# Performance work log

Measured on AMD Instinct MI355X. Metric: run time of the kernel, lower is better.

## Reference

```python
import jax, jax.numpy as jnp
import numpy as np

T, H, I, E, K, L, R = 1024, 1024, 1024, 8, 2, 4, 16
N = 2 * I  # gate_up dim


def setup_inputs() -> dict:
    key = jax.random.key(0)
    ks = jax.random.split(key, 12)
    tw = jax.random.uniform(ks[1], (T, K), dtype=jnp.float32) + 0.1
    tw = tw / tw.sum(axis=-1, keepdims=True)  # routing weights sum to 1
    return {
        "hidden_states": jax.random.normal(ks[0], (T, H), dtype=jnp.float32),
        "topk_weights": tw,
        "w13": jax.random.normal(ks[2], (E, N, H), dtype=jnp.float32) * (1.0 / np.sqrt(H)),
        "w2": jax.random.normal(ks[3], (E, H, I), dtype=jnp.float32) * (1.0 / np.sqrt(I)),
        "gate_up_lora_a": jax.random.normal(ks[4], (L, E, R, H), dtype=jnp.float32) * (1.0 / np.sqrt(H)),
        "gate_up_lora_b": jax.random.normal(ks[5], (L, E, N, R), dtype=jnp.float32) * (1.0 / np.sqrt(R)),
        "down_lora_a": jax.random.normal(ks[6], (L, E, R, I), dtype=jnp.float32) * (1.0 / np.sqrt(I)),
        "down_lora_b": jax.random.normal(ks[7], (L, E, H, R), dtype=jnp.float32) * (1.0 / np.sqrt(R)),
        "scalings": jax.random.uniform(ks[8], (L,), dtype=jnp.float32) + 0.5,
        "topk_ids": jax.random.randint(ks[9], (T, K), 0, E, dtype=jnp.int32),
        "lora_indices": jax.random.randint(ks[10], (T,), 0, L, dtype=jnp.int32),
    }


def reference(hidden_states, topk_weights, w13, w2, gate_up_lora_a,
              gate_up_lora_b, down_lora_a, down_lora_b, scalings,
              topk_ids, lora_indices):
    num_tokens, hidden = hidden_states.shape
    num_experts, gate_up_dim, _ = w13.shape
    top_k = topk_ids.shape[1]
    inter = gate_up_dim // 2
    TKp = num_tokens * top_k

    e_flat = topk_ids.reshape(-1)                      # [TK] expert per dispatched pair
    l_flat = jnp.repeat(lora_indices, top_k)           # [TK] adapter per pair
    w_flat = topk_weights.reshape(-1)                  # [TK] routing weight
    x_rep = jnp.repeat(hidden_states, top_k, axis=0)   # [TK, H]

    # ---- grouped gate_up GEMM (base path): cache1[p] = x[p] @ w13[e(p)]^T ----
    cache1 = jnp.zeros((TKp, gate_up_dim), dtype=hidden_states.dtype)
    for ei in range(num_experts):  # small fixed expert count
        mask = (e_flat == ei)[:, None]
        cache1 = cache1 + jnp.where(mask, x_rep @ w13[ei].T, 0.0)

    # ---- per-expert gate_up LoRA delta, injected BEFORE activation ----
    scal = scalings[l_flat][:, None]                   # [TK, 1]
    Ag = gate_up_lora_a[l_flat, e_flat]                # [TK, R, H]
    Bg = gate_up_lora_b[l_flat, e_flat]                # [TK, N, R]
    tmp = jnp.einsum('prh,ph->pr', Ag, x_rep)
    cache1 = cache1 + jnp.einsum('pnr,pr->pn', Bg, tmp) * scal

    # ---- silu_and_mul on (base + lora) ----
    act = jax.nn.silu(cache1[:, :inter]) * cache1[:, inter:]   # [TK, I]

    # ---- grouped down GEMM (base), routed-weight applied ----
    cache3 = jnp.zeros((TKp, hidden), dtype=hidden_states.dtype)
    for ei in range(num_experts):
        mask = (e_flat == ei)[:, None]
        cache3 = cache3 + jnp.where(mask, act @ w2[ei].T, 0.0)
    cache3 = cache3 * w_flat[:, None]

    # ---- per-expert down LoRA delta (weighted by routing weight) ----
    Ad = down_lora_a[l_flat, e_flat]                   # [TK, R, I]
    Bd = down_lora_b[l_flat, e_flat]                   # [TK, H, R]
    tmpd = jnp.einsum('pri,pi->pr', Ad, act)
    cache3 = cache3 + jnp.einsum('phr,pr->ph', Bd, tmpd) * scal * w_flat[:, None]

    # ---- combine expert outputs (moe_sum over top_k slots) ----
    return cache3.reshape(num_tokens, top_k, hidden).sum(axis=1)
```

## Files before the change

kernel.cpp:

```cpp
#include <hip/hip_runtime.h>
#include <stdint.h>

#define Td 1024
#define Hd 1024
#define Id 1024
#define Ed 8
#define Kd 2
#define Ld 4
#define Rd 16
#define Nd 2048
#define TKd (Td*Kd)

typedef __bf16 bf16x8 __attribute__((ext_vector_type(8)));
typedef float f32x4 __attribute__((ext_vector_type(4)));

__device__ __forceinline__ ushort f2bf(float f) {
    uint32_t u = __builtin_bit_cast(uint32_t, f);
    return (ushort)((u + 0x7fffu + ((u >> 16) & 1u)) >> 16);
}
__device__ __forceinline__ float bf2f(ushort u) {
    uint32_t x = ((uint32_t)u) << 16;
    return __builtin_bit_cast(float, x);
}
__device__ __forceinline__ bf16x8 pack8(float4 a, float4 b) {
    bf16x8 r;
    r[0] = (__bf16)a.x; r[1] = (__bf16)a.y; r[2] = (__bf16)a.z; r[3] = (__bf16)a.w;
    r[4] = (__bf16)b.x; r[5] = (__bf16)b.y; r[6] = (__bf16)b.z; r[7] = (__bf16)b.w;
    return r;
}
__device__ __forceinline__ void cvt16(const float* __restrict__ s, ushort* __restrict__ d) {
    float4 a0 = *(const float4*)(s);
    float4 a1 = *(const float4*)(s + 4);
    float4 a2 = *(const float4*)(s + 8);
    float4 a3 = *(const float4*)(s + 12);
    uint4 o0, o1;
    o0.x = (uint)f2bf(a0.x) | ((uint)f2bf(a0.y) << 16);
    o0.y = (uint)f2bf(a0.z) | ((uint)f2bf(a0.w) << 16);
    o0.z = (uint)f2bf(a1.x) | ((uint)f2bf(a1.y) << 16);
    o0.w = (uint)f2bf(a1.z) | ((uint)f2bf(a1.w) << 16);
    o1.x = (uint)f2bf(a2.x) | ((uint)f2bf(a2.y) << 16);
    o1.y = (uint)f2bf(a2.z) | ((uint)f2bf(a2.w) << 16);
    o1.z = (uint)f2bf(a3.x) | ((uint)f2bf(a3.y) << 16);
    o1.w = (uint)f2bf(a3.z) | ((uint)f2bf(a3.w) << 16);
    *(uint4*)(d) = o0;
    *(uint4*)(d + 8) = o1;
}

#define GLOAD_LDS16(g, l) __builtin_amdgcn_global_load_lds( \
    (const __attribute__((address_space(1))) uint32_t*)(const void*)(g), \
    (__attribute__((address_space(3))) uint32_t*)(void*)(l), 16, 0, 0)

__device__ __forceinline__ int xcd_swz(int bid, int tot) {
    int q = tot >> 3, r = tot & 7;
    int x = bid & 7, i = bid >> 3;
    return (x < r) ? x * (q + 1) + i : r * (q + 1) + (x - r) * q + i;
}

#define TB 2048
#define XB 256
#define CB 384
#define ZB 1024
#define PREP_BLOCKS (TB + XB + CB + ZB + 1)

__global__ __launch_bounds__(256) void k_prep(
    const float* __restrict__ hid,
    const float* __restrict__ gb, const float* __restrict__ db,
    const float* __restrict__ ga, const float* __restrict__ sc,
    const int* __restrict__ tids, const int* __restrict__ lidx,
    ushort* __restrict__ xb,
    ushort* __restrict__ gbbe, ushort* __restrict__ dbbe, ushort* __restrict__ tmp1e,
    float* __restrict__ out, int* __restrict__ sorted, int* __restrict__ offs)
{
    __shared__ float tr[Rd];
    __shared__ int cnt[Ed];
    __shared__ int cur[Ed];
    const int b = blockIdx.x, tid = threadIdx.x;

    if (b < TB) {
        const int p = b;
        const int e = tids[p];
        const int l = lidx[p >> 1];
        const float s = sc[l];
        const int r = tid >> 4, q = tid & 15;
        const float* A = ga + (((size_t)l * Ed + e) * Rd + r) * 1024;
        const float* x = hid + (size_t)(p >> 1) * 1024;
        float sum = 0.f;
        #pragma unroll
        for (int i = 0; i < 16; ++i) {
            int h = q * 4 + 64 * i;
            float4 a = *(const float4*)(A + h);
            float4 v = *(const float4*)(x + h);
            sum += a.x * v.x + a.y * v.y + a.z * v.z + a.w * v.w;
        }
        sum += __shfl_xor(sum, 1); sum += __shfl_xor(sum, 2);
        sum += __shfl_xor(sum, 4); sum += __shfl_xor(sum, 8);
        if (q == 0) tr[r] = sum;
        __syncthreads();
        if (tid < 32) {
            int j0 = tid * 2;
            uint v = 0;
            if ((j0 >> 4) == l)
                v = (uint)f2bf(s * tr[j0 & 15]) | ((uint)f2bf(s * tr[(j0 + 1) & 15]) << 16);
            ((uint*)(tmp1e + (size_t)p * 64))[tid] = v;
        }
    } else if (b < TB + XB) {
        size_t off = ((size_t)(b - TB) * 256 + tid) * 16;
        cvt16(hid + off, xb + off);
    } else if (b < TB + XB + CB) {
        constexpr int GR = Ld * Ed * Nd;
        int i = (b - TB - XB) * 256 + tid;
        const float* src; ushort* dst;
        if (i < GR) {
            int l = i >> 14, e = (i >> 11) & 7, n = i & 2047;
            src = gb + (size_t)i * 16;
            dst = gbbe + ((size_t)(e * Nd + n)) * 64 + l * 16;
        } else {
            int j = i - GR;
            int l = j >> 13, e = (j >> 10) & 7, n = j & 1023;
            src = db + (size_t)j * 16;
            dst = dbbe + ((size_t)(e * Id + n)) * 64 + l * 16;
        }
        cvt16(src, dst);
    } else if (b < TB + XB + CB + ZB) {
        int i = (b - TB - XB - CB) * 256 + tid;
        ((float4*)out)[i] = make_float4(0.f, 0.f, 0.f, 0.f);
    } else {
        if (tid < Ed) cnt[tid] = 0;
        __syncthreads();
        int el[8];
        #pragma unroll
        for (int i = 0; i < 8; ++i) {
            el[i] = tids[tid + i * 256];
            atomicAdd(&cnt[el[i]], 1);
        }
        __syncthreads();
        if (tid == 0) {
            int s = 0;
            for (int e = 0; e < Ed; ++e) { offs[e] = s; cur[e] = s; s += cnt[e]; }
            offs[Ed] = s;
        }
        __syncthreads();
        #pragma unroll
        for (int i = 0; i < 8; ++i) {
            int pos = atomicAdd(&cur[el[i]], 1);
            sorted[pos] = tid + i * 256;
        }
    }
}

__global__ __launch_bounds__(256) void k_tmp_dn(
    const ushort* __restrict__ act, const float* __restrict__ da,
    const float* __restrict__ sc, const int* __restrict__ tids,
    const int* __restrict__ lidx, ushort* __restrict__ tmpde)
{
    const int p = blockIdx.x;
    const int e = tids[p];
    const int l = lidx[p >> 1];
    const float s = sc[l];
    const int tid = threadIdx.x;
    const int r = tid >> 4, q = tid & 15;
    const float* A = da + (((size_t)l * Ed + e) * Rd + r) * 1024;
    const ushort* x = act + (size_t)p * 1024;
    float sum = 0.f;
    #pragma unroll
    for (int i = 0; i < 8; ++i) {
        int h = q * 8 + 128 * i;
        float4 a0 = *(const float4*)(A + h);
        float4 a1 = *(const float4*)(A + h + 4);
        ushort4 v0 = *(const ushort4*)(x + h);
        ushort4 v1 = *(const ushort4*)(x + h + 4);
        sum += a0.x * bf2f(v0.x) + a0.y * bf2f(v0.y) + a0.z * bf2f(v0.z) + a0.w * bf2f(v0.w)
             + a1.x * bf2f(v1.x) + a1.y * bf2f(v1.y) + a1.z * bf2f(v1.z) + a1.w * bf2f(v1.w);
    }
    sum += __shfl_xor(sum, 1); sum += __shfl_xor(sum, 2);
    sum += __shfl_xor(sum, 4); sum += __shfl_xor(sum, 8);
    __shared__ float tr[Rd];
    if (q == 0) tr[r] = sum;
    __syncthreads();
    if (tid < 32) {
        int j0 = tid * 2;
        uint v = 0;
        if ((j0 >> 4) == l)
            v = (uint)f2bf(s * tr[j0 & 15]) | ((uint)f2bf(s * tr[(j0 + 1) & 15]) << 16);
        ((uint*)(tmpde + (size_t)p * 64))[tid] = v;
    }
}

#define GUB 1024
#define W2C 2048

__global__ __launch_bounds__(256) void k_gemm_gu(
    const ushort* __restrict__ xb, const float* __restrict__ w13,
    const ushort* __restrict__ tmp1e, const ushort* __restrict__ gbbe,
    const float* __restrict__ w2, ushort* __restrict__ w2b,
    ushort* __restrict__ act, const int* __restrict__ sorted,
    const int* __restrict__ offs)
{
    __shared__ ushort As[2][64][32];
    __shared__ ushort Bs[2][128][32];
    const int tid = threadIdx.x;

    if (blockIdx.x >= GUB) {
        size_t off = ((size_t)(blockIdx.x - GUB) * 256 + tid) * 16;
        cvt16(w2 + off, w2b + off);
        return;
    }

    const int lane = tid & 63, wave = tid >> 6;
    const int wr = wave >> 1, wc = wave & 1;
    const int fr = lane & 15, fk = (lane >> 4) * 8;

    int off[Ed + 1];
    #pragma unroll
    for (int e = 0; e <= Ed; ++e) off[e] = offs[e];
    int mt[Ed], pre[Ed + 1];
    pre[0] = 0;
    #pragma unroll
    for (int e = 0; e < Ed; ++e) {
        mt[e] = (off[e + 1] - off[e] + 63) / 64;
        pre[e + 1] = pre[e] + mt[e] * 16;
    }
    const int tot = pre[Ed];

    for (int bid = blockIdx.x; bid < tot; bid += GUB) {
        const int tau = xcd_swz(bid, tot);
        int e = 0;
        while (tau >= pre[e + 1]) ++e;
        int local = tau - pre[e];
        int nt = local / mt[e];
        int mtile = local - nt * mt[e];
        const int m0 = off[e] + mtile * 64;
        const int mend = off[e + 1];
        const int n0 = nt * 64;

        const ushort *asrc, *aesrc;
        {
            int aIdx = m0 + (tid >> 2); if (aIdx > mend - 1) aIdx = mend - 1;
            int p = sorted[aIdx];
            asrc  = xb + (size_t)(p >> 1) * 1024 + (tid & 3) * 8;
            aesrc = tmp1e + (size_t)p * 64 + (tid & 3) * 8;
        }
        const int brow = tid >> 1, bhalf = tid & 1;
        const int bg_row = (brow < 64) ? (n0 + brow) : (1024 + n0 + brow - 64);
        const float* bsrc = w13 + ((size_t)e * Nd + bg_row) * 1024 + bhalf * 16;
        const ushort* besrc[2];
        #pragma unroll
        for (int r = 0; r < 2; ++r) {
            int c = r * 256 + tid;
            int row = c >> 2, kc = c & 3;
            int grow = (row < 64) ? (n0 + row) : (1024 + n0 + row - 64);
            besrc[r] = gbbe + ((size_t)e * Nd + grow) * 64 + kc * 8;
        }

        f32x4 ag[2][2] = {}, au[2][2] = {};
        auto step = [&](int b) {
            bf16x8 af[2], bg[2], bu[2];
            #pragma unroll
            for (int mi = 0; mi < 2; ++mi)
                af[mi] = *(const bf16x8*)(&As[b][wr * 32 + mi * 16 + fr][fk]);
            #pragma unroll
            for (int ni = 0; ni < 2; ++ni) {
                bg[ni] = *(const bf16x8*)(&Bs[b][wc * 32 + ni * 16 + fr][fk]);
                bu[ni] = *(const bf16x8*)(&Bs[b][64 + wc * 32 + ni * 16 + fr][fk]);
            }
            #pragma unroll
            for (int mi = 0; mi < 2; ++mi)
                #pragma unroll
                for (int ni = 0; ni < 2; ++ni) {
                    ag[mi][ni] = __builtin_amdgcn_mfma_f32_16x16x32_bf16(af[mi], bg[ni], ag[mi][ni], 0, 0, 0);
                    au[mi][ni] = __builtin_amdgcn_mfma_f32_16x16x32_bf16(af[mi], bu[ni], au[mi][ni], 0, 0, 0);
                }
        };

        GLOAD_LDS16(asrc, (char*)&As[0][0][0] + (wave * 64) * 16);
        {
            float4 y0 = *(const float4*)(bsrc);
            float4 y1 = *(const float4*)(bsrc + 4);
            float4 y2 = *(const float4*)(bsrc + 8);
            float4 y3 = *(const float4*)(bsrc + 12);
            *(bf16x8*)(&Bs[0][brow][bhalf * 16])     = pack8(y0, y1);
            *(bf16x8*)(&Bs[0][brow][bhalf * 16 + 8]) = pack8(y2, y3);
        }
        __syncthreads();

        int buf = 0;
        for (int k0 = 32; k0 < 1024; k0 += 32) {
            GLOAD_LDS16(asrc + k0, (char*)&As[buf ^ 1][0][0] + (wave * 64) * 16);
            float4 y0 = *(const float4*)(bsrc + k0);
            float4 y1 = *(const float4*)(bsrc + k0 + 4);
            float4 y2 = *(const float4*)(bsrc + k0 + 8);
            float4 y3 = *(const float4*)(bsrc + k0 + 12);

            step(buf);

            *(bf16x8*)(&Bs[buf ^ 1][brow][bhalf * 16])     = pack8(y0, y1);
            *(bf16x8*)(&Bs[buf ^ 1][brow][bhalf * 16 + 8]) = pack8(y2, y3);
            __syncthreads();
            buf ^= 1;
        }
        step(buf);

        #pragma unroll
        for (int es = 0; es < 2; ++es) {
            GLOAD_LDS16(aesrc + es * 32, (char*)&As[es][0][0] + (wave * 64) * 16);
            #pragma unroll
            for (int r = 0; r < 2; ++r)
                GLOAD_LDS16(besrc[r] + es * 32, (char*)&Bs[es][0][0] + (r * 256 + wave * 64) * 16);
            __syncthreads();
            step(es);
        }

        const int rb = wr * 32 + (lane >> 4) * 4;
        #pragma unroll
        for (int mi = 0; mi < 2; ++mi) {
            #pragma unroll
            for (int j = 0; j < 4; ++j) {
                int sidx = m0 + rb + mi * 16 + j;
                if (sidx < mend) {
                    int p = sorted[sidx];
                    ushort* ar = act + (size_t)p * 1024 + n0 + wc * 32;
                    #pragma unroll
                    for (int ni = 0; ni < 2; ++ni) {
                        float g = ag[mi][ni][j], u = au[mi][ni][j];
                        float v = g / (1.f + __expf(-g)) * u;
                        ar[ni * 16 + fr] = f2bf(v);
                    }
                }
            }
        }
        __syncthreads();
    }
}

__global__ __launch_bounds__(256) void k_gemm_dn(
    const ushort* __restrict__ act, const ushort* __restrict__ w2b,
    const ushort* __restrict__ tmpde, const ushort* __restrict__ dbbe,
    const float* __restrict__ tw, float* __restrict__ out,
    const int* __restrict__ sorted, const int* __restrict__ offs)
{
    __shared__ ushort As[64][32];
    __shared__ ushort Bs[64][32];
    const int tid = threadIdx.x, lane = tid & 63, wave = tid >> 6;
    const int wr = wave >> 1, wc = wave & 1;
    const int fr = lane & 15, fk = (lane >> 4) * 8;

    int off[Ed + 1];
    #pragma unroll
    for (int e = 0; e <= Ed; ++e) off[e] = offs[e];
    int mt[Ed], pre[Ed + 1];
    pre[0] = 0;
    #pragma unroll
    for (int e = 0; e < Ed; ++e) {
        mt[e] = (off[e + 1] - off[e] + 63) / 64;
        pre[e + 1] = pre[e] + mt[e] * 16;
    }
    const int tot = pre[Ed];

    for (int bid = blockIdx.x; bid < tot; bid += gridDim.x) {
        const int tau = xcd_swz(bid, tot);
        int e = 0;
        while (tau >= pre[e + 1]) ++e;
        int local = tau - pre[e];
        int nt = local / mt[e];
        int mtile = local - nt * mt[e];
        const int m0 = off[e] + mtile * 64;
        const int mend = off[e + 1];
        const int n0 = nt * 64;

        const ushort *asrc, *aesrc, *bsrc, *besrc;
        {
            int aIdx = m0 + (tid >> 2); if (aIdx > mend - 1) aIdx = mend - 1;
            int p = sorted[aIdx];
            asrc  = act + (size_t)p * 1024 + (tid & 3) * 8;
            aesrc = tmpde + (size_t)p * 64 + (tid & 3) * 8;
            int row = tid >> 2, kc = tid & 3;
            bsrc  = w2b + ((size_t)e * Hd + n0 + row) * 1024 + kc * 8;
            besrc = dbbe + ((size_t)e * Hd + n0 + row) * 64 + kc * 8;
        }

        f32x4 acc[2][2] = {};
        auto step = [&]() {
            bf16x8 af[2], bv[2];
            #pragma unroll
            for (int mi = 0; mi < 2; ++mi)
                af[mi] = *(const bf16x8*)(&As[wr * 32 + mi * 16 + fr][fk]);
            #pragma unroll
            for (int ni = 0; ni < 2; ++ni)
                bv[ni] = *(const bf16x8*)(&Bs[wc * 32 + ni * 16 + fr][fk]);
            #pragma unroll
            for (int mi = 0; mi < 2; ++mi)
                #pragma unroll
                for (int ni = 0; ni < 2; ++ni)
                    acc[mi][ni] = __builtin_amdgcn_mfma_f32_16x16x32_bf16(af[mi], bv[ni], acc[mi][ni], 0, 0, 0);
        };

        for (int k0 = 0; k0 < 1024; k0 += 32) {
            GLOAD_LDS16(asrc + k0, (char*)&As[0][0] + (wave * 64) * 16);
            GLOAD_LDS16(bsrc + k0, (char*)&Bs[0][0] + (wave * 64) * 16);
            __syncthreads();
            step();
            __syncthreads();
        }
        #pragma unroll
        for (int es = 0; es < 2; ++es) {
            GLOAD_LDS16(aesrc + es * 32, (char*)&As[0][0] + (wave * 64) * 16);
            GLOAD_LDS16(besrc + es * 32, (char*)&Bs[0][0] + (wave * 64) * 16);
            __syncthreads();
            step();
            __syncthreads();
        }

        const int rb = wr * 32 + (lane >> 4) * 4;
        #pragma unroll
        for (int mi = 0; mi < 2; ++mi) {
            #pragma unroll
            for (int j = 0; j < 4; ++j) {
                int sidx = m0 + rb + mi * 16 + j;
                if (sidx < mend) {
                    int p = sorted[sidx];
                    float w = tw[p];
                    float* orow = out + (size_t)(p >> 1) * 1024 + n0 + wc * 32;
                    #pragma unroll
                    for (int ni = 0; ni < 2; ++ni)
                        atomicAdd(&orow[ni * 16 + fr], w * acc[mi][ni][j]);
                }
            }
        }
    }
}

extern "C" void kernel_launch(void* const* d_in, const int* in_sizes, int n_in,
                              void* d_out, int out_size, void* d_ws, size_t ws_size,
                              hipStream_t stream) {
    const float* hid  = (const float*)d_in[0];
    const float* tw   = (const float*)d_in[1];
    const float* w13  = (const float*)d_in[2];
    const float* w2   = (const float*)d_in[3];
    const float* ga   = (const float*)d_in[4];
    const float* gb   = (const float*)d_in[5];
    const float* da   = (const float*)d_in[6];
    const float* db   = (const float*)d_in[7];
    const float* sc   = (const float*)d_in[8];
    const int*   tids = (const int*)d_in[9];
    const int*   lidx = (const int*)d_in[10];
    float* out = (float*)d_out;

    char* ws = (char*)d_ws;
    ushort* xb     = (ushort*)(ws);
    ushort* w2b    = (ushort*)(ws + (2ull  << 20));
    ushort* gbbe   = (ushort*)(ws + (18ull << 20));
    ushort* dbbe   = (ushort*)(ws + (20ull << 20));
    ushort* tmp1e  = (ushort*)(ws + (21ull << 20));
    ushort* tmpde  = (ushort*)(ws + (21ull << 20) + (256u << 10));
    ushort* act    = (ushort*)(ws + (22ull << 20));
    int*    sorted = (int*)(ws + (26ull << 20));
    int*    offs   = (int*)(ws + (26ull << 20) + TKd * 4);

    k_prep<<<PREP_BLOCKS, 256, 0, stream>>>(hid, gb, db, ga, sc, tids, lidx,
                                            xb, gbbe, dbbe, tmp1e, out, sorted, offs);
    k_gemm_gu<<<GUB + W2C, 256, 0, stream>>>(xb, w13, tmp1e, gbbe, w2, w2b, act, sorted, offs);
    k_tmp_dn<<<TKd, 256, 0, stream>>>(act, da, sc, tids, lidx, tmpde);
    k_gemm_dn<<<1024, 256, 0, stream>>>(act, w2b, tmpde, dbbe, tw, out, sorted, offs);
}
```

Baseline: 89.26 us.

## Split-K the gate_up GEMM in two with atomic fp32 accumulation and separate SiLU kernel

The grouped gate_up GEMM now splits K=1024 into two halves processed by different blocks, doubling tile count for better occupancy. Partial results are atomically added into a new fp32 cache1 buffer (zeroed in the prep kernel), and the SiLU-and-mul epilogue moves to a new elementwise kernel that writes bf16 act. This trades extra zeroing, fp32 atomic traffic over a 16 MB buffer, and an additional launch for more parallelism.

```diff
diff --git a/kernel.cpp b/kernel.cpp
--- a/kernel.cpp
+++ b/kernel.cpp
@@ -60,7 +60,8 @@
 #define XB 256
 #define CB 384
 #define ZB 1024
-#define PREP_BLOCKS (TB + XB + CB + ZB + 1)
+#define ZC 4096
+#define PREP_BLOCKS (TB + XB + CB + ZB + ZC + 1)
 
 __global__ __launch_bounds__(256) void k_prep(
     const float* __restrict__ hid,
@@ -69,7 +70,8 @@
     const int* __restrict__ tids, const int* __restrict__ lidx,
     ushort* __restrict__ xb,
     ushort* __restrict__ gbbe, ushort* __restrict__ dbbe, ushort* __restrict__ tmp1e,
-    float* __restrict__ out, int* __restrict__ sorted, int* __restrict__ offs)
+    float* __restrict__ out, float* __restrict__ cache1,
+    int* __restrict__ sorted, int* __restrict__ offs)
 {
     __shared__ float tr[Rd];
     __shared__ int cnt[Ed];
@@ -124,6 +126,9 @@
     } else if (b < TB + XB + CB + ZB) {
         int i = (b - TB - XB - CB) * 256 + tid;
         ((float4*)out)[i] = make_float4(0.f, 0.f, 0.f, 0.f);
+    } else if (b < TB + XB + CB + ZB + ZC) {
+        int i = (b - TB - XB - CB - ZB) * 256 + tid;
+        ((float4*)cache1)[i] = make_float4(0.f, 0.f, 0.f, 0.f);
     } else {
         if (tid < Ed) cnt[tid] = 0;
         __syncthreads();
@@ -146,6 +151,22 @@
             sorted[pos] = tid + i * 256;
         }
     }
+}
+
+__global__ __launch_bounds__(256) void k_silu(const float* __restrict__ c1, ushort* __restrict__ act) {
+    int i = blockIdx.x * blockDim.x + threadIdx.x;
+    int p = i >> 8;
+    int c = (i & 255) * 4;
+    float4 g = *reinterpret_cast<const float4*>(&c1[(size_t)p * Nd + c]);
+    float4 u = *reinterpret_cast<const float4*>(&c1[(size_t)p * Nd + Id + c]);
+    float r0 = g.x / (1.f + __expf(-g.x)) * u.x;
+    float r1 = g.y / (1.f + __expf(-g.y)) * u.y;
+    float r2 = g.z / (1.f + __expf(-g.z)) * u.z;
+    float r3 = g.w / (1.f + __expf(-g.w)) * u.w;
+    uint2 o;
+    o.x = (uint)f2bf(r0) | ((uint)f2bf(r1) << 16);
+    o.y = (uint)f2bf(r2) | ((uint)f2bf(r3) << 16);
+    *reinterpret_cast<uint2*>(&act[(size_t)p * Id + c]) = o;
 }
 
 __global__ __launch_bounds__(256) void k_tmp_dn(
@@ -193,7 +214,7 @@
     const ushort* __restrict__ xb, const float* __restrict__ w13,
     const ushort* __restrict__ tmp1e, const ushort* __restrict__ gbbe,
     const float* __restrict__ w2, ushort* __restrict__ w2b,
-    ushort* __restrict__ act, const int* __restrict__ sorted,
+    float* __restrict__ cache1, const int* __restrict__ sorted,
     const int* __restrict__ offs)
 {
     __shared__ ushort As[2][64][32];
@@ -220,10 +241,12 @@
         mt[e] = (off[e + 1] - off[e] + 63) / 64;
         pre[e + 1] = pre[e] + mt[e] * 16;
     }
-    const int tot = pre[Ed];
-
-    for (int bid = blockIdx.x; bid < tot; bid += GUB) {
-        const int tau = xcd_swz(bid, tot);
+    const int tot2 = pre[Ed] * 2;
+
+    for (int bid = blockIdx.x; bid < tot2; bid += GUB) {
+        int tau = xcd_swz(bid, tot2);
+        const int ks = tau & 1;
+        tau >>= 1;
         int e = 0;
         while (tau >= pre[e + 1]) ++e;
         int local = tau - pre[e];
@@ -232,6 +255,7 @@
         const int m0 = off[e] + mtile * 64;
         const int mend = off[e + 1];
         const int n0 = nt * 64;
+        const int kbase = ks * 512;
 
         const ushort *asrc, *aesrc;
         {
@@ -272,19 +296,19 @@
                 }
         };
 
-        GLOAD_LDS16(asrc, (char*)&As[0][0][0] + (wave * 64) * 16);
+        GLOAD_LDS16(asrc + kbase, (char*)&As[0][0][0] + (wave * 64) * 16);
         {
-            float4 y0 = *(const float4*)(bsrc);
-            float4 y1 = *(const float4*)(bsrc + 4);
-            float4 y2 = *(const float4*)(bsrc + 8);
-            float4 y3 = *(const float4*)(bsrc + 12);
+            float4 y0 = *(const float4*)(bsrc + kbase);
+            float4 y1 = *(const float4*)(bsrc + kbase + 4);
+            float4 y2 = *(const float4*)(bsrc + kbase + 8);
+            float4 y3 = *(const float4*)(bsrc + kbase + 12);
             *(bf16x8*)(&Bs[0][brow][bhalf * 16])     = pack8(y0, y1);
             *(bf16x8*)(&Bs[0][brow][bhalf * 16 + 8]) = pack8(y2, y3);
         }
         __syncthreads();
 
         int buf = 0;
-        for (int k0 = 32; k0 < 1024; k0 += 32) {
+        for (int k0 = kbase + 32; k0 < kbase + 512; k0 += 32) {
             GLOAD_LDS16(asrc + k0, (char*)&As[buf ^ 1][0][0] + (wave * 64) * 16);
             float4 y0 = *(const float4*)(bsrc + k0);
             float4 y1 = *(const float4*)(bsrc + k0 + 4);
@@ -300,14 +324,16 @@
         }
         step(buf);
 
-        #pragma unroll
-        for (int es = 0; es < 2; ++es) {
-            GLOAD_LDS16(aesrc + es * 32, (char*)&As[es][0][0] + (wave * 64) * 16);
-            #pragma unroll
-            for (int r = 0; r < 2; ++r)
-                GLOAD_LDS16(besrc[r] + es * 32, (char*)&Bs[es][0][0] + (r * 256 + wave * 64) * 16);
-            __syncthreads();
-            step(es);
+        if (ks == 0) {
+            #pragma unroll
+            for (int es = 0; es < 2; ++es) {
+                GLOAD_LDS16(aesrc + es * 32, (char*)&As[es][0][0] + (wave * 64) * 16);
+                #pragma unroll
+                for (int r = 0; r < 2; ++r)
+                    GLOAD_LDS16(besrc[r] + es * 32, (char*)&Bs[es][0][0] + (r * 256 + wave * 64) * 16);
+                __syncthreads();
+                step(es);
+            }
         }
 
         const int rb = wr * 32 + (lane >> 4) * 4;
@@ -318,12 +344,11 @@
                 int sidx = m0 + rb + mi * 16 + j;
                 if (sidx < mend) {
                     int p = sorted[sidx];
-                    ushort* ar = act + (size_t)p * 1024 + n0 + wc * 32;
+                    float* cr = cache1 + (size_t)p * Nd + n0 + wc * 32;
                     #pragma unroll
                     for (int ni = 0; ni < 2; ++ni) {
-                        float g = ag[mi][ni][j], u = au[mi][ni][j];
-                        float v = g / (1.f + __expf(-g)) * u;
-                        ar[ni * 16 + fr] = f2bf(v);
+                        atomicAdd(&cr[ni * 16 + fr], ag[mi][ni][j]);
+                        atomicAdd(&cr[Id + ni * 16 + fr], au[mi][ni][j]);
                     }
                 }
             }
@@ -453,12 +478,14 @@
     ushort* tmp1e  = (ushort*)(ws + (21ull << 20));
     ushort* tmpde  = (ushort*)(ws + (21ull << 20) + (256u << 10));
     ushort* act    = (ushort*)(ws + (22ull << 20));
-    int*    sorted = (int*)(ws + (26ull << 20));
-    int*    offs   = (int*)(ws + (26ull << 20) + TKd * 4);
+    float*  cache1 = (float*)(ws + (26ull << 20));
+    int*    sorted = (int*)(ws + (42ull << 20));
+    int*    offs   = (int*)(ws + (42ull << 20) + TKd * 4);
 
     k_prep<<<PREP_BLOCKS, 256, 0, stream>>>(hid, gb, db, ga, sc, tids, lidx,
-                                            xb, gbbe, dbbe, tmp1e, out, sorted, offs);
-    k_gemm_gu<<<GUB + W2C, 256, 0, stream>>>(xb, w13, tmp1e, gbbe, w2, w2b, act, sorted, offs);
+                                            xb, gbbe, dbbe, tmp1e, out, cache1, sorted, offs);
+    k_gemm_gu<<<GUB + W2C, 256, 0, stream>>>(xb, w13, tmp1e, gbbe, w2, w2b, cache1, sorted, offs);
+    k_silu<<<(TKd * Id / 4) / 256, 256, 0, stream>>>(cache1, act);
     k_tmp_dn<<<TKd, 256, 0, stream>>>(act, da, sc, tids, lidx, tmpde);
     k_gemm_dn<<<1024, 256, 0, stream>>>(act, w2b, tmpde, dbbe, tw, out, sorted, offs);
 }
```

Measured after the change: 116.7 us. 30.7% more time.
